# Kernel tuning notes

Measured on AMD Instinct MI355X. Metric: run time of the kernel, lower is better.

## Reference

```python
import jax, jax.numpy as jnp
import numpy as np

NEG = -9e15  # matches -9000000000000000.0 in the torch source


def setup_inputs() -> dict:
    key = jax.random.key(0)
    k1, k2, k3, k4 = jax.random.split(key, 4)
    N, F_in, F_out = 8192, 512, 64
    h = jax.random.normal(k1, (N, F_in), dtype=jnp.float32)
    adj = jax.random.randint(k2, (N, N), 0, 2, dtype=jnp.int32)
    # xavier_uniform with gain=1.414
    def xavier(k, shape, gain=1.414):
        fan_in, fan_out = shape[0], shape[1]
        bound = gain * np.sqrt(6.0 / (fan_in + fan_out))
        return jax.random.uniform(k, shape, dtype=jnp.float32, minval=-bound, maxval=bound)
    W = xavier(k3, (F_in, F_out))
    a = xavier(k4, (2 * F_out, 1))
    return {"h": h, "adj": adj, "W": W, "a": a}


def reference(h, adj, W, a):
    alpha = 0.2
    F_out = W.shape[1]
    Wh = h.astype(jnp.float32) @ W                      # [N, F_out]
    # e[i,j] = leakyrelu( Wh[i] . a[:F_out] + Wh[j] . a[F_out:] )
    Wh1 = Wh @ a[:F_out, :]                             # [N, 1]
    Wh2 = Wh @ a[F_out:, :]                             # [N, 1]
    e = jax.nn.leaky_relu(Wh1 + Wh2.T, negative_slope=alpha)  # [N, N]
    scores = jnp.where(adj > 0, e, NEG)                 # mask non-edges
    attention = jax.nn.softmax(scores, axis=1)          # row softmax
    h_prime = attention @ Wh                            # [N, F_out]
    return h_prime
```

## Files before the change

### kernel.cpp

```cpp
#include <hip/hip_runtime.h>
#include <cstdint>
#include <cstddef>


#define GAT_N    8192
#define GAT_FIN  512
#define GAT_F    64
#define TJ       64
#define JSPLIT   4
#define JCHUNK   (GAT_N / JSPLIT)
#define NTILES   (JCHUNK / TJ)

__device__ __forceinline__ float lrelu(float x) { return fmaxf(x, 0.2f * x); }

__device__ __forceinline__ unsigned enc_f32(float f) {
    unsigned b = __float_as_uint(f);
    return b ^ ((b & 0x80000000u) ? 0xFFFFFFFFu : 0x80000000u);
}
__device__ __forceinline__ float dec_f32(unsigned u) {
    return __uint_as_float(u ^ ((u & 0x80000000u) ? 0x80000000u : 0xFFFFFFFFu));
}

__device__ __forceinline__ void gload_lds16(const void* g, void* l) {
    __builtin_amdgcn_global_load_lds(
        (const __attribute__((address_space(1))) void*)g,
        (__attribute__((address_space(3))) void*)l, 16, 0, 0);
}

__global__ __launch_bounds__(256) void k_wh(
    const float* __restrict__ h, const float* __restrict__ W,
    const float* __restrict__ a,
    float* __restrict__ Wh, float* __restrict__ wh1, float* __restrict__ wh2,
    unsigned int* __restrict__ mw2)
{
    __shared__ float sW[2][128 * GAT_F];
    __shared__ unsigned int smax[16];
    const int tid = threadIdx.x;
    const int w   = tid >> 6;
    const size_t r0 = (size_t)blockIdx.x * 16;
    const int rp = tid >> 4;
    const int f4 = (tid & 15) * 4;

    const char* wsrc = (const char*)W;
    {
        char* dst = (char*)sW[0];
#pragma unroll
        for (int i = 0; i < 8; ++i)
            gload_lds16(wsrc + (size_t)(tid + i * 256) * 16,
                        dst + (size_t)(w * 64 + i * 256) * 16);
    }

    const float* ha = h + (r0 + rp) * GAT_FIN;
    float4 acc = {0.f, 0.f, 0.f, 0.f};

    for (int c = 0; c < 4; ++c) {
        __syncthreads();
        if (c + 1 < 4) {
            const char* src = wsrc + (size_t)(c + 1) * (128 * GAT_F * 4);
            char* dst = (char*)sW[(c + 1) & 1];
#pragma unroll
            for (int i = 0; i < 8; ++i)
                gload_lds16(src + (size_t)(tid + i * 256) * 16,
                            dst + (size_t)(w * 64 + i * 256) * 16);
        }
        const float* wc = sW[c & 1];
#pragma unroll 4
        for (int k4 = 0; k4 < 32; ++k4) {
            float4 hv = *(const float4*)&ha[c * 128 + k4 * 4];
            const float* hvf = (const float*)&hv;
#pragma unroll
            for (int kk = 0; kk < 4; ++kk) {
                float4 wv = *(const float4*)&wc[(k4 * 4 + kk) * GAT_F + f4];
                acc.x = fmaf(hvf[kk], wv.x, acc.x);
                acc.y = fmaf(hvf[kk], wv.y, acc.y);
                acc.z = fmaf(hvf[kk], wv.z, acc.z);
                acc.w = fmaf(hvf[kk], wv.w, acc.w);
            }
        }
    }

    *(float4*)&Wh[(r0 + rp) * GAT_F + f4] = acc;

    float4 a1 = *(const float4*)&a[f4];
    float4 a2 = *(const float4*)&a[GAT_F + f4];
    float pa = acc.x*a1.x + acc.y*a1.y + acc.z*a1.z + acc.w*a1.w;
    float pb = acc.x*a2.x + acc.y*a2.y + acc.z*a2.z + acc.w*a2.w;
#pragma unroll
    for (int m = 1; m < 16; m <<= 1) {
        pa += __shfl_xor(pa, m);
        pb += __shfl_xor(pb, m);
    }
    if ((tid & 15) == 0) {
        wh1[r0 + rp] = pa;
        wh2[r0 + rp] = pb;
        smax[rp] = enc_f32(pb);
    }
    __syncthreads();
    if (tid == 0) {
        unsigned m = smax[0];
#pragma unroll
        for (int r = 1; r < 16; ++r) m = max(m, smax[r]);
        atomicMax(mw2, m);
    }
}

__global__ __launch_bounds__(256, 2) void k_attend(
    const int* __restrict__ adj, const float* __restrict__ Wh,
    const float* __restrict__ wh1, const float* __restrict__ wh2,
    const unsigned int* __restrict__ mw2,
    float* __restrict__ po, float* __restrict__ pl)
{
    __shared__ float sWh[2][TJ * GAT_F];
    __shared__ float sP[4][8][TJ];

    const int tid  = threadIdx.x;
    const int w    = tid >> 6;
    const int lane = tid & 63;
    const int rw   = blockIdx.x * 32 + w * 8;
    const int j0   = blockIdx.y * JCHUNK;

    const float Mw2 = dec_f32(*mw2);

    const int rA   = lane >> 4;
    const int jsub = (lane & 15) * 4;
    const float a0 = wh1[rw + rA];
    const float a4 = wh1[rw + rA + 4];
    const float M0 = lrelu(a0 + Mw2);
    const float M4 = lrelu(a4 + Mw2);

    const int jb = lane >> 3, fb = lane & 7;
    const int wrow0 = jb * 8 * GAT_F;
    const int g0o = (((2 * fb)    ) ^ jb) * 4;
    const int g1o = (((2 * fb) + 1) ^ jb) * 4;

    int soff[4];
#pragma unroll
    for (int c = 0; c < 4; ++c) {
        int G = tid + c * 256;
        int j = G >> 4, gp = G & 15;
        soff[c] = (j * 16 + (gp ^ (j >> 3))) * 16;
    }
    const int ldsoff = w * 64 * 16;

    const char* wsrcb = (const char*)(Wh + (size_t)j0 * GAT_F);

    const int* ap0 = adj + (size_t)(rw + rA) * GAT_N + j0 + jsub;
    const int* ap4 = ap0 + (size_t)4 * GAT_N;
    const float* b4p = wh2 + j0 + jsub;

    {
        char* dstb = (char*)sWh[0];
#pragma unroll
        for (int c = 0; c < 4; ++c)
            gload_lds16(wsrcb + soff[c], dstb + ldsoff + c * 256 * 16);
    }
    int4  adjc0 = *(const int4*)ap0;
    int4  adjc4 = *(const int4*)ap4;
    float4 b4c  = *(const float4*)b4p;

    float4 oacc[8][2] = {};
    float l0 = 0.f, l4 = 0.f;

    for (int t = 0; t < NTILES; ++t) {
        const int cur = t & 1;
        __syncthreads();

        const int nstep = (t + 1 < NTILES) ? (t + 1) * TJ : t * TJ;
        int4  adjn0 = *(const int4*)(ap0 + nstep);
        int4  adjn4 = *(const int4*)(ap4 + nstep);
        float4 b4n  = *(const float4*)(b4p + nstep);
        if (t + 1 < NTILES) {
            const char* src = wsrcb + (size_t)(t + 1) * (TJ * GAT_F * 4);
            char* dstb = (char*)sWh[cur ^ 1];
#pragma unroll
            for (int c = 0; c < 4; ++c)
                gload_lds16(src + soff[c], dstb + ldsoff + c * 256 * 16);
        }

        float4 p0, p4;
        p0.x = adjc0.x > 0 ? __expf(lrelu(a0 + b4c.x) - M0) : 0.f;
        p0.y = adjc0.y > 0 ? __expf(lrelu(a0 + b4c.y) - M0) : 0.f;
        p0.z = adjc0.z > 0 ? __expf(lrelu(a0 + b4c.z) - M0) : 0.f;
        p0.w = adjc0.w > 0 ? __expf(lrelu(a0 + b4c.w) - M0) : 0.f;
        p4.x = adjc4.x > 0 ? __expf(lrelu(a4 + b4c.x) - M4) : 0.f;
        p4.y = adjc4.y > 0 ? __expf(lrelu(a4 + b4c.y) - M4) : 0.f;
        p4.z = adjc4.z > 0 ? __expf(lrelu(a4 + b4c.z) - M4) : 0.f;
        p4.w = adjc4.w > 0 ? __expf(lrelu(a4 + b4c.w) - M4) : 0.f;
        l0 += p0.x + p0.y + p0.z + p0.w;
        l4 += p4.x + p4.y + p4.z + p4.w;
        *(float4*)&sP[w][rA][jsub]     = p0;
        *(float4*)&sP[w][rA + 4][jsub] = p4;
        __builtin_amdgcn_wave_barrier();

        const float* swc = sWh[cur];
        const float* pb  = &sP[w][0][jb * 8];
#pragma unroll
        for (int jh = 0; jh < 2; ++jh) {
            float4 wv0[4], wv1[4];
#pragma unroll
            for (int jj = 0; jj < 4; ++jj) {
                const int jr = wrow0 + (jh * 4 + jj) * GAT_F;
                wv0[jj] = *(const float4*)&swc[jr + g0o];
                wv1[jj] = *(const float4*)&swc[jr + g1o];
            }
#pragma unroll
            for (int r = 0; r < 8; ++r) {
                float4 pq = *(const float4*)&pb[r * TJ + jh * 4];
                const float* pf = (const float*)&pq;
#pragma unroll
                for (int jj = 0; jj < 4; ++jj) {
                    oacc[r][0].x = fmaf(pf[jj], wv0[jj].x, oacc[r][0].x);
                    oacc[r][0].y = fmaf(pf[jj], wv0[jj].y, oacc[r][0].y);
                    oacc[r][0].z = fmaf(pf[jj], wv0[jj].z, oacc[r][0].z);
                    oacc[r][0].w = fmaf(pf[jj], wv0[jj].w, oacc[r][0].w);
                    oacc[r][1].x = fmaf(pf[jj], wv1[jj].x, oacc[r][1].x);
                    oacc[r][1].y = fmaf(pf[jj], wv1[jj].y, oacc[r][1].y);
                    oacc[r][1].z = fmaf(pf[jj], wv1[jj].z, oacc[r][1].z);
                    oacc[r][1].w = fmaf(pf[jj], wv1[jj].w, oacc[r][1].w);
                }
            }
        }

        adjc0 = adjn0; adjc4 = adjn4; b4c = b4n;
    }

#pragma unroll
    for (int m = 1; m < 16; m <<= 1) {
        l0 += __shfl_xor(l0, m);
        l4 += __shfl_xor(l4, m);
    }
    if ((lane & 15) == 0) {
        pl[(size_t)blockIdx.y * GAT_N + rw + rA]     = l0;
        pl[(size_t)blockIdx.y * GAT_N + rw + rA + 4] = l4;
    }

    const size_t obase = ((size_t)blockIdx.y * GAT_N + rw) * GAT_F + fb * 8;
#pragma unroll
    for (int r = 0; r < 8; ++r) {
#pragma unroll
        for (int hh = 0; hh < 2; ++hh) {
            float4 v = oacc[r][hh];
#pragma unroll
            for (int m = 8; m <= 32; m <<= 1) {
                v.x += __shfl_xor(v.x, m);
                v.y += __shfl_xor(v.y, m);
                v.z += __shfl_xor(v.z, m);
                v.w += __shfl_xor(v.w, m);
            }
            if (jb == 0)
                *(float4*)&po[obase + (size_t)r * GAT_F + hh * 4] = v;
        }
    }
}

__global__ __launch_bounds__(256) void k_merge(
    const float* __restrict__ po, const float* __restrict__ pl,
    float* __restrict__ out)
{
    const int idx = blockIdx.x * 256 + threadIdx.x;
    const int i = idx >> 6;
    float s = 0.f, ls = 0.f;
#pragma unroll
    for (int y = 0; y < JSPLIT; ++y) {
        s  += po[(size_t)y * GAT_N * GAT_F + idx];
        ls += pl[(size_t)y * GAT_N + i];
    }
    out[idx] = s / ls;
}

extern "C" void kernel_launch(void* const* d_in, const int* in_sizes, int n_in,
                              void* d_out, int out_size, void* d_ws, size_t ws_size,
                              hipStream_t stream) {
    (void)in_sizes; (void)n_in; (void)out_size; (void)ws_size;
    const float* h   = (const float*)d_in[0];
    const int*   adj = (const int*)d_in[1];
    const float* W   = (const float*)d_in[2];
    const float* a   = (const float*)d_in[3];
    float* out = (float*)d_out;

    float* ws  = (float*)d_ws;
    float* Wh  = ws;
    float* wh1 = ws + 524288;
    float* wh2 = ws + 532480;
    unsigned int* mw2 = (unsigned int*)(ws + 540672);
    float* po  = ws + 548864;
    float* pl  = ws + 2646016;

    hipMemsetAsync(mw2, 0, 4, stream);
    k_wh    <<<GAT_N / 16, 256, 0, stream>>>(h, W, a, Wh, wh1, wh2, mw2);
    k_attend<<<dim3(GAT_N / 32, JSPLIT), 256, 0, stream>>>(adj, Wh, wh1, wh2, mw2, po, pl);
    k_merge <<<GAT_N * GAT_F / 256, 256, 0, stream>>>(po, pl, out);
}
```

Measured before the change: 459.6 us.

## Use split-bf16 MFMA for attention-weighted aggregation with transposed bf16 Wh

Replaces the FP32 FMA-based P·Wh product in the attention kernel with bf16 MFMA 16x16x32 instructions. Three products (hi·hi, lo·hi, hi·lo) approximate fp32 accuracy. The Wh projection kernel now writes Wh transposed as hi/lo bf16 pairs instead of fp32, and the attention kernel processes 64 rows per block with occupancy raised to 3. The goal is to move the dominant aggregation work onto matrix cores. The cost is extra conversion work and some precision loss from truncating bf16 splits.

```diff
diff --git a/kernel.cpp b/kernel.cpp
--- a/kernel.cpp
+++ b/kernel.cpp
@@ -11,6 +11,9 @@
 #define JCHUNK   (GAT_N / JSPLIT)
 #define NTILES   (JCHUNK / TJ)
 
+typedef __attribute__((ext_vector_type(8))) short short8;
+typedef __attribute__((ext_vector_type(4))) float f32x4;
+
 __device__ __forceinline__ float lrelu(float x) { return fmaxf(x, 0.2f * x); }
 
 __device__ __forceinline__ unsigned enc_f32(float f) {
@@ -19,6 +22,12 @@
 }
 __device__ __forceinline__ float dec_f32(unsigned u) {
     return __uint_as_float(u ^ ((u & 0x80000000u) ? 0x80000000u : 0xFFFFFFFFu));
+}
+__device__ __forceinline__ short f2bf_trunc(float f) {
+    return (short)(__float_as_uint(f) >> 16);
+}
+__device__ __forceinline__ float bfhi(float f) {
+    return __uint_as_float(__float_as_uint(f) & 0xFFFF0000u);
 }
 
 __device__ __forceinline__ void gload_lds16(const void* g, void* l) {
@@ -30,13 +39,15 @@
 __global__ __launch_bounds__(256) void k_wh(
     const float* __restrict__ h, const float* __restrict__ W,
     const float* __restrict__ a,
-    float* __restrict__ Wh, float* __restrict__ wh1, float* __restrict__ wh2,
-    unsigned int* __restrict__ mw2)
+    float* __restrict__ wh1, float* __restrict__ wh2,
+    unsigned int* __restrict__ mw2,
+    unsigned short* __restrict__ whtHi, unsigned short* __restrict__ whtLo)
 {
-    __shared__ float sW[2][128 * GAT_F];
+    __shared__ float sW[2][64 * GAT_F];
+    __shared__ unsigned short sTh[GAT_F][16];
+    __shared__ unsigned short sTl[GAT_F][16];
     __shared__ unsigned int smax[16];
     const int tid = threadIdx.x;
-    const int w   = tid >> 6;
     const size_t r0 = (size_t)blockIdx.x * 16;
     const int rp = tid >> 4;
     const int f4 = (tid & 15) * 4;
@@ -45,32 +56,32 @@
     {
         char* dst = (char*)sW[0];
 #pragma unroll
-        for (int i = 0; i < 8; ++i)
-            gload_lds16(wsrc + (size_t)(tid + i * 256) * 16,
-                        dst + (size_t)(w * 64 + i * 256) * 16);
+        for (int c = 0; c < 4; ++c)
+            gload_lds16(wsrc + (size_t)(tid + c * 256) * 16,
+                        dst + (size_t)(tid + c * 256) * 16);
     }
 
     const float* ha = h + (r0 + rp) * GAT_FIN;
     float4 acc = {0.f, 0.f, 0.f, 0.f};
 
-    for (int c = 0; c < 4; ++c) {
+    for (int ck = 0; ck < 8; ++ck) {
         __syncthreads();
-        if (c + 1 < 4) {
-            const char* src = wsrc + (size_t)(c + 1) * (128 * GAT_F * 4);
-            char* dst = (char*)sW[(c + 1) & 1];
-#pragma unroll
-            for (int i = 0; i < 8; ++i)
-                gload_lds16(src + (size_t)(tid + i * 256) * 16,
-                            dst + (size_t)(w * 64 + i * 256) * 16);
-        }
-        const float* wc = sW[c & 1];
+        if (ck + 1 < 8) {
+            const char* src = wsrc + (size_t)(ck + 1) * 16384;
+            char* dst = (char*)sW[(ck + 1) & 1];
+#pragma unroll
+            for (int c = 0; c < 4; ++c)
+                gload_lds16(src + (size_t)(tid + c * 256) * 16,
+                            dst + (size_t)(tid + c * 256) * 16);
+        }
+        const float* wcp = sW[ck & 1];
 #pragma unroll 4
-        for (int k4 = 0; k4 < 32; ++k4) {
-            float4 hv = *(const float4*)&ha[c * 128 + k4 * 4];
+        for (int k4 = 0; k4 < 16; ++k4) {
+            float4 hv = *(const float4*)&ha[ck * 64 + k4 * 4];
             const float* hvf = (const float*)&hv;
 #pragma unroll
             for (int kk = 0; kk < 4; ++kk) {
-                float4 wv = *(const float4*)&wc[(k4 * 4 + kk) * GAT_F + f4];
+                float4 wv = *(const float4*)&wcp[(k4 * 4 + kk) * GAT_F + f4];
                 acc.x = fmaf(hvf[kk], wv.x, acc.x);
                 acc.y = fmaf(hvf[kk], wv.y, acc.y);
                 acc.z = fmaf(hvf[kk], wv.z, acc.z);
@@ -79,8 +90,6 @@
         }
     }
 
-    *(float4*)&Wh[(r0 + rp) * GAT_F + f4] = acc;
-
     float4 a1 = *(const float4*)&a[f4];
     float4 a2 = *(const float4*)&a[GAT_F + f4];
     float pa = acc.x*a1.x + acc.y*a1.y + acc.z*a1.z + acc.w*a1.w;
@@ -95,7 +104,23 @@
         wh2[r0 + rp] = pb;
         smax[rp] = enc_f32(pb);
     }
+
+    const float* af = (const float*)&acc;
+#pragma unroll
+    for (int e = 0; e < 4; ++e) {
+        float v = af[e];
+        sTh[f4 + e][rp] = (unsigned short)f2bf_trunc(v);
+        sTl[f4 + e][rp] = (unsigned short)f2bf_trunc(v - bfhi(v));
+    }
     __syncthreads();
+
+    {
+        const int f = tid >> 2, rq = tid & 3;
+        uint2 vh = *(const uint2*)&sTh[f][rq * 4];
+        uint2 vl = *(const uint2*)&sTl[f][rq * 4];
+        *(uint2*)&whtHi[(size_t)f * GAT_N + r0 + rq * 4] = vh;
+        *(uint2*)&whtLo[(size_t)f * GAT_N + r0 + rq * 4] = vl;
+    }
     if (tid == 0) {
         unsigned m = smax[0];
 #pragma unroll
@@ -104,152 +129,126 @@
     }
 }
 
-__global__ __launch_bounds__(256, 2) void k_attend(
-    const int* __restrict__ adj, const float* __restrict__ Wh,
+__global__ __launch_bounds__(256, 3) void k_attend(
+    const int* __restrict__ adj,
+    const unsigned short* __restrict__ whtHi,
+    const unsigned short* __restrict__ whtLo,
     const float* __restrict__ wh1, const float* __restrict__ wh2,
     const unsigned int* __restrict__ mw2,
     float* __restrict__ po, float* __restrict__ pl)
 {
-    __shared__ float sWh[2][TJ * GAT_F];
-    __shared__ float sP[4][8][TJ];
+    __shared__ char sB[2][16384];
 
     const int tid  = threadIdx.x;
     const int w    = tid >> 6;
     const int lane = tid & 63;
-    const int rw   = blockIdx.x * 32 + w * 8;
+    const int fl   = lane & 15;
+    const int jg   = lane >> 4;
+    const int rw   = blockIdx.x * 64 + w * 16;
     const int j0   = blockIdx.y * JCHUNK;
 
     const float Mw2 = dec_f32(*mw2);
-
-    const int rA   = lane >> 4;
-    const int jsub = (lane & 15) * 4;
-    const float a0 = wh1[rw + rA];
-    const float a4 = wh1[rw + rA + 4];
-    const float M0 = lrelu(a0 + Mw2);
-    const float M4 = lrelu(a4 + Mw2);
-
-    const int jb = lane >> 3, fb = lane & 7;
-    const int wrow0 = jb * 8 * GAT_F;
-    const int g0o = (((2 * fb)    ) ^ jb) * 4;
-    const int g1o = (((2 * fb) + 1) ^ jb) * 4;
-
-    int soff[4];
+    const float ai  = wh1[rw + fl];
+    const float Mi  = lrelu(ai + Mw2);
+
+    const char* ssrc[4]; int sdst[4];
 #pragma unroll
     for (int c = 0; c < 4; ++c) {
-        int G = tid + c * 256;
-        int j = G >> 4, gp = G & 15;
-        soff[c] = (j * 16 + (gp ^ (j >> 3))) * 16;
-    }
-    const int ldsoff = w * 64 * 16;
-
-    const char* wsrcb = (const char*)(Wh + (size_t)j0 * GAT_F);
-
-    const int* ap0 = adj + (size_t)(rw + rA) * GAT_N + j0 + jsub;
-    const int* ap4 = ap0 + (size_t)4 * GAT_N;
-    const float* b4p = wh2 + j0 + jsub;
+        int G = tid + (c & 1) * 256;
+        int f = G >> 3, g = G & 7;
+        const unsigned short* base = (c < 2) ? whtHi : whtLo;
+        ssrc[c] = (const char*)(base + (size_t)f * GAT_N + j0 + ((g ^ (f & 7)) * 8));
+        sdst[c] = ((c < 2) ? 0 : 8192) + G * 16;
+    }
+
+    const int off0 = fl * 128 + (((0 * 4 + jg) ^ (fl & 7)) * 16);
+    const int off1 = fl * 128 + (((1 * 4 + jg) ^ (fl & 7)) * 16);
+
+    const int*   ap = adj + (size_t)(rw + fl) * GAT_N + j0 + jg * 8;
+    const float* wp = wh2 + j0 + jg * 8;
 
     {
-        char* dstb = (char*)sWh[0];
 #pragma unroll
         for (int c = 0; c < 4; ++c)
-            gload_lds16(wsrcb + soff[c], dstb + ldsoff + c * 256 * 16);
-    }
-    int4  adjc0 = *(const int4*)ap0;
-    int4  adjc4 = *(const int4*)ap4;
-    float4 b4c  = *(const float4*)b4p;
-
-    float4 oacc[8][2] = {};
-    float l0 = 0.f, l4 = 0.f;
+            gload_lds16(ssrc[c], (char*)sB[0] + sdst[c]);
+    }
+    int4 ac[4]; float4 wc[4];
+#pragma unroll
+    for (int q = 0; q < 4; ++q) {
+        int o = (q >> 1) * 32 + (q & 1) * 4;
+        ac[q] = *(const int4*)(ap + o);
+        wc[q] = *(const float4*)(wp + o);
+    }
+
+    f32x4 acc[4] = {};
+    float psum = 0.f;
 
     for (int t = 0; t < NTILES; ++t) {
         const int cur = t & 1;
         __syncthreads();
 
-        const int nstep = (t + 1 < NTILES) ? (t + 1) * TJ : t * TJ;
-        int4  adjn0 = *(const int4*)(ap0 + nstep);
-        int4  adjn4 = *(const int4*)(ap4 + nstep);
-        float4 b4n  = *(const float4*)(b4p + nstep);
         if (t + 1 < NTILES) {
-            const char* src = wsrcb + (size_t)(t + 1) * (TJ * GAT_F * 4);
-            char* dstb = (char*)sWh[cur ^ 1];
 #pragma unroll
             for (int c = 0; c < 4; ++c)
-                gload_lds16(src + soff[c], dstb + ldsoff + c * 256 * 16);
-        }
-
-        float4 p0, p4;
-        p0.x = adjc0.x > 0 ? __expf(lrelu(a0 + b4c.x) - M0) : 0.f;
-        p0.y = adjc0.y > 0 ? __expf(lrelu(a0 + b4c.y) - M0) : 0.f;
-        p0.z = adjc0.z > 0 ? __expf(lrelu(a0 + b4c.z) - M0) : 0.f;
-        p0.w = adjc0.w > 0 ? __expf(lrelu(a0 + b4c.w) - M0) : 0.f;
-        p4.x = adjc4.x > 0 ? __expf(lrelu(a4 + b4c.x) - M4) : 0.f;
-        p4.y = adjc4.y > 0 ? __expf(lrelu(a4 + b4c.y) - M4) : 0.f;
-        p4.z = adjc4.z > 0 ? __expf(lrelu(a4 + b4c.z) - M4) : 0.f;
-        p4.w = adjc4.w > 0 ? __expf(lrelu(a4 + b4c.w) - M4) : 0.f;
-        l0 += p0.x + p0.y + p0.z + p0.w;
-        l4 += p4.x + p4.y + p4.z + p4.w;
-        *(float4*)&sP[w][rA][jsub]     = p0;
-        *(float4*)&sP[w][rA + 4][jsub] = p4;
-        __builtin_amdgcn_wave_barrier();
-
-        const float* swc = sWh[cur];
-        const float* pb  = &sP[w][0][jb * 8];
-#pragma unroll
-        for (int jh = 0; jh < 2; ++jh) {
-            float4 wv0[4], wv1[4];
-#pragma unroll
-            for (int jj = 0; jj < 4; ++jj) {
-                const int jr = wrow0 + (jh * 4 + jj) * GAT_F;
-                wv0[jj] = *(const float4*)&swc[jr + g0o];
-                wv1[jj] = *(const float4*)&swc[jr + g1o];
-            }
-#pragma unroll
-            for (int r = 0; r < 8; ++r) {
-                float4 pq = *(const float4*)&pb[r * TJ + jh * 4];
-                const float* pf = (const float*)&pq;
-#pragma unroll
-                for (int jj = 0; jj < 4; ++jj) {
-                    oacc[r][0].x = fmaf(pf[jj], wv0[jj].x, oacc[r][0].x);
-                    oacc[r][0].y = fmaf(pf[jj], wv0[jj].y, oacc[r][0].y);
-                    oacc[r][0].z = fmaf(pf[jj], wv0[jj].z, oacc[r][0].z);
-                    oacc[r][0].w = fmaf(pf[jj], wv0[jj].w, oacc[r][0].w);
-                    oacc[r][1].x = fmaf(pf[jj], wv1[jj].x, oacc[r][1].x);
-                    oacc[r][1].y = fmaf(pf[jj], wv1[jj].y, oacc[r][1].y);
-                    oacc[r][1].z = fmaf(pf[jj], wv1[jj].z, oacc[r][1].z);
-                    oacc[r][1].w = fmaf(pf[jj], wv1[jj].w, oacc[r][1].w);
+                gload_lds16(ssrc[c] + (size_t)(t + 1) * 128,
+                            (char*)sB[cur ^ 1] + sdst[c]);
+        }
+        const int tn = (t + 1 < NTILES) ? t + 1 : t;
+        int4 an[4]; float4 wn[4];
+#pragma unroll
+        for (int q = 0; q < 4; ++q) {
+            int o = tn * TJ + (q >> 1) * 32 + (q & 1) * 4;
+            an[q] = *(const int4*)(ap + o);
+            wn[q] = *(const float4*)(wp + o);
+        }
+
+        const char* sbc = sB[cur];
+#pragma unroll
+        for (int s = 0; s < 2; ++s) {
+            float pv[8];
+#pragma unroll
+            for (int hh = 0; hh < 2; ++hh) {
+                const int*   avi = (const int*)&ac[s * 2 + hh];
+                const float* bvf = (const float*)&wc[s * 2 + hh];
+#pragma unroll
+                for (int e = 0; e < 4; ++e) {
+                    float sc = lrelu(ai + bvf[e]);
+                    float pe = __expf(sc - Mi);
+                    pv[hh * 4 + e] = (avi[e] > 0) ? pe : 0.f;
                 }
             }
-        }
-
-        adjc0 = adjn0; adjc4 = adjn4; b4c = b4n;
-    }
-
-#pragma unroll
-    for (int m = 1; m < 16; m <<= 1) {
-        l0 += __shfl_xor(l0, m);
-        l4 += __shfl_xor(l4, m);
-    }
-    if ((lane & 15) == 0) {
-        pl[(size_t)blockIdx.y * GAT_N + rw + rA]     = l0;
-        pl[(size_t)blockIdx.y * GAT_N + rw + rA + 4] = l4;
-    }
-
-    const size_t obase = ((size_t)blockIdx.y * GAT_N + rw) * GAT_F + fb * 8;
-#pragma unroll
-    for (int r = 0; r < 8; ++r) {
-#pragma unroll
-        for (int hh = 0; hh < 2; ++hh) {
-            float4 v = oacc[r][hh];
-#pragma unroll
-            for (int m = 8; m <= 32; m <<= 1) {
-                v.x += __shfl_xor(v.x, m);
-                v.y += __shfl_xor(v.y, m);
-                v.z += __shfl_xor(v.z, m);
-                v.w += __shfl_xor(v.w, m);
-            }
-            if (jb == 0)
-                *(float4*)&po[obase + (size_t)r * GAT_F + hh * 4] = v;
-        }
+            short8 ph, plo;
+#pragma unroll
+            for (int e = 0; e < 8; ++e) {
+                psum  += pv[e];
+                ph[e]  = f2bf_trunc(pv[e]);
+                plo[e] = f2bf_trunc(pv[e] - bfhi(pv[e]));
+            }
+            const int offs = s ? off1 : off0;
+#pragma unroll
+            for (int nb = 0; nb < 4; ++nb) {
+                short8 bh = *(const short8*)(sbc + offs + nb * 2048);
+                short8 bl = *(const short8*)(sbc + 8192 + offs + nb * 2048);
+                acc[nb] = __builtin_amdgcn_mfma_f32_16x16x32_bf16(ph,  bh, acc[nb], 0, 0, 0);
+                acc[nb] = __builtin_amdgcn_mfma_f32_16x16x32_bf16(plo, bh, acc[nb], 0, 0, 0);
+                acc[nb] = __builtin_amdgcn_mfma_f32_16x16x32_bf16(ph,  bl, acc[nb], 0, 0, 0);
+            }
+        }
+#pragma unroll
+        for (int q = 0; q < 4; ++q) { ac[q] = an[q]; wc[q] = wn[q]; }
+    }
+
+    psum += __shfl_xor(psum, 16);
+    psum += __shfl_xor(psum, 32);
+    if (lane < 16)
+        pl[(size_t)blockIdx.y * GAT_N + rw + lane] = psum;
+
+    const size_t ob = ((size_t)blockIdx.y * GAT_N + rw + jg * 4) * GAT_F + fl;
+#pragma unroll
+    for (int nb = 0; nb < 4; ++nb) {
+#pragma unroll
+        for (int r = 0; r < 4; ++r)
+            po[ob + (size_t)r * GAT_F + nb * 16] = acc[nb][r];
     }
 }
 
@@ -278,16 +277,18 @@
     const float* a   = (const float*)d_in[3];
     float* out = (float*)d_out;
 
-    float* ws  = (float*)d_ws;
-    float* Wh  = ws;
-    float* wh1 = ws + 524288;
-    float* wh2 = ws + 532480;
-    unsigned int* mw2 = (unsigned int*)(ws + 540672);
-    float* po  = ws + 548864;
-    float* pl  = ws + 2646016;
+    char* wsb = (char*)d_ws;
+    float*          wh1   = (float*)(wsb);
+    float*          wh2   = (float*)(wsb + 32768);
+    unsigned int*   mw2   = (unsigned int*)(wsb + 65536);
+    unsigned short* whtHi = (unsigned short*)(wsb + 131072);
+    unsigned short* whtLo = (unsigned short*)(wsb + 1179648);
+    float*          po    = (float*)(wsb + 2228224);
+    float*          pl    = (float*)(wsb + 10616832);
 
     hipMemsetAsync(mw2, 0, 4, stream);
-    k_wh    <<<GAT_N / 16, 256, 0, stream>>>(h, W, a, Wh, wh1, wh2, mw2);
-    k_attend<<<dim3(GAT_N / 32, JSPLIT), 256, 0, stream>>>(adj, Wh, wh1, wh2, mw2, po, pl);
+    k_wh    <<<GAT_N / 16, 256, 0, stream>>>(h, W, a, wh1, wh2, mw2, whtHi, whtLo);
+    k_attend<<<dim3(GAT_N / 64, JSPLIT), 256, 0, stream>>>(adj, whtHi, whtLo,
+                                                           wh1, wh2, mw2, po, pl);
     k_merge <<<GAT_N * GAT_F / 256, 256, 0, stream>>>(po, pl, out);
 }
```

After: 427.4 us. 7.0% less time.
